# Performance work log

Measured on AMD Instinct MI355X. Metric: run time of the kernel, lower is better.

The kernel has to match this reference:

```python
import jax, jax.numpy as jnp
import numpy as np

B, S, H, L, V, T = 128, 512, 512, 2, 30, 64  # batch, enc len, hidden, layers, vocab, decode len


def _p(k, shape):
    return jax.random.normal(k, shape, jnp.float32) * 0.05


def setup_inputs() -> dict:
    key = jax.random.key(0)
    ks = jax.random.split(key, 24)
    inp = {"x": jax.random.normal(ks[0], (B, S, 2), jnp.float32)}
    inp["emb"] = _p(ks[1], (V, H))
    # encoder GRU (input dim 2 for layer 0, H for layer 1); PyTorch gate order r,z,n
    inp["enc_Wih0"] = _p(ks[2], (3 * H, 2));  inp["enc_Whh0"] = _p(ks[3], (3 * H, H))
    inp["enc_bih0"] = _p(ks[4], (3 * H,));    inp["enc_bhh0"] = _p(ks[5], (3 * H,))
    inp["enc_Wih1"] = _p(ks[6], (3 * H, H));  inp["enc_Whh1"] = _p(ks[7], (3 * H, H))
    inp["enc_bih1"] = _p(ks[8], (3 * H,));    inp["enc_bhh1"] = _p(ks[9], (3 * H,))
    # decoder GRU (input dim H)
    inp["dec_Wih0"] = _p(ks[10], (3 * H, H)); inp["dec_Whh0"] = _p(ks[11], (3 * H, H))
    inp["dec_bih0"] = _p(ks[12], (3 * H,));   inp["dec_bhh0"] = _p(ks[13], (3 * H,))
    inp["dec_Wih1"] = _p(ks[14], (3 * H, H)); inp["dec_Whh1"] = _p(ks[15], (3 * H, H))
    inp["dec_bih1"] = _p(ks[16], (3 * H,));   inp["dec_bhh1"] = _p(ks[17], (3 * H,))
    inp["fc_W"] = _p(ks[18], (V, 2 * H));     inp["fc_b"] = _p(ks[19], (V,))
    return inp


def gru_cell(xt, h, Wih, Whh, bih, bhh):
    gi = xt @ Wih.T + bih
    gh = h @ Whh.T + bhh
    i_r, i_z, i_n = jnp.split(gi, 3, axis=-1)
    h_r, h_z, h_n = jnp.split(gh, 3, axis=-1)
    r = jax.nn.sigmoid(i_r + h_r)
    z = jax.nn.sigmoid(i_z + h_z)
    n = jnp.tanh(i_n + r * h_n)
    return (1.0 - z) * n + z * h


def _forward(x, emb,
             enc_Wih0, enc_Whh0, enc_bih0, enc_bhh0,
             enc_Wih1, enc_Whh1, enc_bih1, enc_bhh1,
             dec_Wih0, dec_Whh0, dec_bih0, dec_bhh0,
             dec_Wih1, dec_Whh1, dec_bih1, dec_bhh1,
             fc_W, fc_b):
    b = x.shape[0]
    h0 = jnp.zeros((b, H), x.dtype)

    # ---- encoder: 2-layer GRU scanned over time ----
    def enc_step(hs, xt):
        a = gru_cell(xt, hs[0], enc_Wih0, enc_Whh0, enc_bih0, enc_bhh0)
        c = gru_cell(a, hs[1], enc_Wih1, enc_Whh1, enc_bih1, enc_bhh1)
        return (a, c), c

    (e0, e1), out_enc_t = jax.lax.scan(enc_step, (h0, h0), x.transpose(1, 0, 2))
    out_enc = out_enc_t.transpose(1, 0, 2)  # [B, S, H]

    def dec_step(carry, _):
        (d0, d1), tok = carry
        e = emb[tok]  # [B, H]
        n0 = gru_cell(e, d0, dec_Wih0, dec_Whh0, dec_bih0, dec_bhh0)
        n1 = gru_cell(n0, d1, dec_Wih1, dec_Whh1, dec_bih1, dec_bhh1)
        out_dec = n1  # [B, H]
        sim = jnp.einsum('bsh,bh->bs', out_enc, out_dec)  # [B, S]
        # faithful to nn.Softmax() implicit dim on 3-D [B,S,1] tensor -> dim=0 (batch)
        att_w = jax.nn.softmax(sim, axis=0)
        attention = jnp.einsum('bs,bsh->bh', att_w, out_enc)  # [B, H]
        logits = jnp.concatenate([out_dec, attention], axis=-1) @ fc_W.T + fc_b  # [B, V]
        tok_next = jnp.argmax(logits, axis=-1)
        return ((n0, n1), tok_next), logits

    tok0 = jnp.zeros((b,), jnp.int32)
    ((f0, f1), _), logits_t = jax.lax.scan(dec_step, ((e0, e1), tok0), None, length=T)
    vec_out = logits_t.transpose(1, 0, 2)  # [B, T, V]
    hidden = jnp.stack([f0, f1], axis=0)   # [n_layers, B, H]
    return vec_out, hidden


def reference(x, emb,
              enc_Wih0, enc_Whh0, enc_bih0, enc_bhh0,
              enc_Wih1, enc_Whh1, enc_bih1, enc_bhh1,
              dec_Wih0, dec_Whh0, dec_bih0, dec_bhh0,
              dec_Wih1, dec_Whh1, dec_bih1, dec_bhh1,
              fc_W, fc_b):
    return _forward(x, emb,
                    enc_Wih0, enc_Whh0, enc_bih0, enc_bhh0,
                    enc_Wih1, enc_Whh1, enc_bih1, enc_bhh1,
                    dec_Wih0, dec_Whh0, dec_bih0, dec_bhh0,
                    dec_Wih1, dec_Whh1, dec_bih1, dec_bhh1,
                    fc_W, fc_b)
```

## Files before the change

kernel.cpp:

```cpp
#include <hip/hip_runtime.h>
#include <math.h>

typedef short  s16x8 __attribute__((ext_vector_type(8)));
typedef float  f32x4 __attribute__((ext_vector_type(4)));
typedef unsigned short u16;
typedef unsigned long long u64;

#define MFMA16(a, b, c) __builtin_amdgcn_mfma_f32_16x16x32_bf16((a), (b), (c), 0, 0, 0)

#define BB 128
#define SS 512
#define HH 512
#define VV 30
#define TT 64

#define SC_SYS  __HIP_MEMORY_SCOPE_SYSTEM

__device__ __forceinline__ float b2f(u16 v) {
  union { unsigned int u; float f; } c; c.u = ((unsigned int)v) << 16; return c.f;
}
__device__ __forceinline__ u16 f2b(float f) {
  union { float f; unsigned int u; } c; c.f = f;
  unsigned int r = (c.u + 0x7FFFu + ((c.u >> 16) & 1u)) >> 16;
  return (u16)r;
}
__device__ __forceinline__ float sigm(float x) { return 1.f / (1.f + expf(-x)); }
__device__ __forceinline__ s16x8 ldf(const u16* p) { return *(const s16x8*)p; }

__device__ __forceinline__ u64  ld64c(const u64* p)      { return __hip_atomic_load(p, __ATOMIC_RELAXED, SC_SYS); }
__device__ __forceinline__ void st16c(u16* p, u16 v)     { __hip_atomic_store(p, v, __ATOMIC_RELAXED, SC_SYS); }
__device__ __forceinline__ void stf32c(float* p, float v){ __hip_atomic_store(p, v, __ATOMIC_RELAXED, SC_SYS); }
__device__ __forceinline__ float ldf32c(const float* p)  { return __hip_atomic_load(p, __ATOMIC_RELAXED, SC_SYS); }
__device__ __forceinline__ void sti32c(int* p, int v)    { __hip_atomic_store(p, v, __ATOMIC_RELAXED, SC_SYS); }
__device__ __forceinline__ int  ldi32c(const int* p)     { return __hip_atomic_load(p, __ATOMIC_RELAXED, SC_SYS); }

__device__ unsigned int g_cnt[8];
__device__ float g_smx[SS], g_ssum[SS];

#define C_L0 0
#define C_L1 1
#define C_G0 2
#define C_G1 3
#define C_SIM 4
#define C_SMX 5
#define C_ATT 6

__device__ __forceinline__ void waitp(int idx, int target) {
  if (target <= 0) return;
  unsigned long long t0 = __builtin_amdgcn_s_memrealtime();
  while ((int)__hip_atomic_load(&g_cnt[idx], __ATOMIC_RELAXED, SC_SYS) < target) {
    __builtin_amdgcn_s_sleep(1);
    if (__builtin_amdgcn_s_memrealtime() - t0 > (1ull << 21)) break;
  }
}
__device__ __forceinline__ void waitc2(int i1, int t1, int i2, int t2) {
  if (threadIdx.x == 0) { waitp(i1, t1); waitp(i2, t2); }
  __syncthreads();
}
__device__ __forceinline__ void waitc3(int i1, int t1, int i2, int t2, int i3, int t3) {
  if (threadIdx.x == 0) { waitp(i1, t1); waitp(i2, t2); waitp(i3, t3); }
  __syncthreads();
}
__device__ __forceinline__ void waitc4(int i1, int t1, int i2, int t2, int i3, int t3, int i4, int t4) {
  if (threadIdx.x == 0) { waitp(i1, t1); waitp(i2, t2); waitp(i3, t3); waitp(i4, t4); }
  __syncthreads();
}
__device__ __forceinline__ void arrive(int idx) {
  __syncthreads();
  if (threadIdx.x == 0) {
    asm volatile("s_waitcnt vmcnt(0) lgkmcnt(0)" ::: "memory");
    __hip_atomic_fetch_add(&g_cnt[idx], 1u, __ATOMIC_RELAXED, SC_SYS);
  }
}

__device__ __forceinline__ s16x8 ldl(const u16* SM, int row, int slot) {
  return *(const s16x8*)&SM[(row << 8) + ((slot ^ (row & 15)) << 3)];
}

__device__ __forceinline__ void stage64(u16* SMb, const u16* SRC, int mbase, int kc) {
  const int t = threadIdx.x;
  const u64* base = (const u64*)SRC;
  u64 v[16];
#pragma unroll
  for (int j = 0; j < 16; ++j) {
    const int g = kc * 8 + (j >> 1);
    const int half = j & 1;
    v[j] = ld64c(base + (size_t)(g * 128 + mbase + half * 32) * 8 + t);
  }
#pragma unroll
  for (int j = 0; j < 16; ++j) {
    const int gl = j >> 1, half = j & 1;
    const int row = half * 32 + (t >> 3);
    const int w = t & 7;
    const int s = ((w & 4) << 2) + 2 * gl + ((w >> 1) & 1);
    *(u64*)&SMb[(row << 8) + ((s ^ (row & 15)) << 3) + ((w & 1) << 2)] = v[j];
  }
}

__device__ __forceinline__ void stage128(u16* SM, const u16* SRC, int kc) {
  const int t = threadIdx.x;
  const u64* base = (const u64*)SRC;
  u64 v[32];
#pragma unroll
  for (int j = 0; j < 32; ++j) {
    const int g = kc * 8 + (j >> 2);
    const int q = j & 3;
    v[j] = ld64c(base + (size_t)(g * 128 + q * 32) * 8 + t);
  }
#pragma unroll
  for (int j = 0; j < 32; ++j) {
    const int gl = j >> 2, q = j & 3;
    const int row = q * 32 + (t >> 3);
    const int w = t & 7;
    const int s = ((w & 4) << 2) + 2 * gl + ((w >> 1) & 1);
    *(u64*)&SM[(row << 8) + ((s ^ (row & 15)) << 3) + ((w & 1) << 2)] = v[j];
  }
}


template <bool GATHER, bool COH_H>
__device__ __forceinline__ void gru_dual_staged(
    int bx, u16* SM,
    const u16* __restrict__ A1s, const int* __restrict__ gather,
    const u16* __restrict__ A2s,
    const u16* __restrict__ Wihs, const u16* __restrict__ Whhs,
    const float* __restrict__ bih, const float* __restrict__ bhh,
    float* __restrict__ hf, u16* __restrict__ hs_new,
    u16* __restrict__ oe, size_t oe_mstride)
{
  const int tid  = threadIdx.x;
  const int wave = tid >> 6, lane = tid & 63;
  const int lrow = lane & 15, lq = lane >> 4;
  const int gidx = bx >> 1;
  const int j0 = gidx * 16;
  const int mbase = (bx & 1) * 64;
  const int lr = wave * 16 + lrow;
  const int m0 = mbase + wave * 16;

  const u16* a1p = nullptr;
  if (GATHER)
    a1p = A1s + (size_t)ldi32c(&gather[m0 + lrow]) * 1024 + lq * 8;

  const u16* bp[6];
#pragma unroll
  for (int t = 0; t < 6; ++t) {
    int g = (t < 3) ? t : t - 3;
    const u16* W = (t < 3) ? Wihs : Whhs;
    bp[t] = W + (size_t)(g * HH + j0 + lrow) * 1024 + lq * 8;
  }

  f32x4 acc[6];
#pragma unroll
  for (int t = 0; t < 6; ++t) acc[t] = (f32x4){0.f, 0.f, 0.f, 0.f};

  for (int kc = 0; kc < 4; ++kc) {
    if (!GATHER) stage64(SM, A1s, mbase, kc);
    stage64(SM + 64 * 256, A2s, mbase, kc);
    __syncthreads();
#pragma unroll
    for (int ki = 0; ki < 4; ++ki) {
      const int sl = ki * 4 + lq;
      s16x8 a1h, a1l;
      if (GATHER) { a1h = ldf(a1p); a1l = ldf(a1p + 512); a1p += 32; }
      else        { a1h = ldl(SM, lr, sl); a1l = ldl(SM, lr, 16 + sl); }
      s16x8 a2h = ldl(SM, 64 + lr, sl), a2l = ldl(SM, 64 + lr, 16 + sl);
#pragma unroll
      for (int t = 0; t < 6; ++t) {
        s16x8 bh = ldf(bp[t]), bl = ldf(bp[t] + 512); bp[t] += 32;
        s16x8 ah = (t < 3) ? a1h : a2h;
        s16x8 al = (t < 3) ? a1l : a2l;
        acc[t] = MFMA16(ah, bh, acc[t]);
        acc[t] = MFMA16(ah, bl, acc[t]);
        acc[t] = MFMA16(al, bh, acc[t]);
      }
    }
    __syncthreads();
  }

  const int c = j0 + lrow;
  const float bir = bih[c], biz = bih[HH + c], bin = bih[2 * HH + c];
  const float bhr = bhh[c], bhz = bhh[HH + c], bhn = bhh[2 * HH + c];
#pragma unroll
  for (int r = 0; r < 4; ++r) {
    int m = mbase + wave * 16 + lq * 4 + r;
    float ir = acc[0][r] + bir, iz = acc[1][r] + biz, inn = acc[2][r] + bin;
    float hr = acc[3][r] + bhr, hz = acc[4][r] + bhz, hn = acc[5][r] + bhn;
    float rr = sigm(ir + hr);
    float zz = sigm(iz + hz);
    float nn = tanhf(inn + rr * hn);
    float hp = COH_H ? ldf32c(&hf[(size_t)m * HH + c]) : hf[(size_t)m * HH + c];
    float hv = (1.f - zz) * nn + zz * hp;
    if (COH_H) stf32c(&hf[(size_t)m * HH + c], hv);
    else       hf[(size_t)m * HH + c] = hv;
    u16 hi = f2b(hv);
    size_t cb = (size_t)(gidx * 128 + m) * 32 + lrow;
    st16c(&hs_new[cb], hi);
    st16c(&hs_new[cb + 16], f2b(hv - b2f(hi)));
    if (oe) oe[(size_t)m * oe_mstride + c] = hi;
  }
}

__device__ __forceinline__ void gru_l0_staged(
    int bx, int p, u16* SM,
    const float* __restrict__ x, const float* __restrict__ Wih0,
    const u16* __restrict__ Whh0s,
    const float* __restrict__ bih0, const float* __restrict__ bhh0,
    const u16* __restrict__ As,
    float* __restrict__ af, u16* __restrict__ as_new)
{
  const int tid  = threadIdx.x;
  const int wave = tid >> 6, lane = tid & 63;
  const int lrow = lane & 15, lq = lane >> 4;
  const int j0 = bx * 16;
  const int mw = wave * 32;
  const int r0 = mw + lrow, r1 = mw + 16 + lrow;

  const u16* bp[3];
#pragma unroll
  for (int t = 0; t < 3; ++t)
    bp[t] = Whh0s + (size_t)(t * HH + j0 + lrow) * 1024 + lq * 8;

  f32x4 acc[2][3];
#pragma unroll
  for (int i = 0; i < 2; ++i)
#pragma unroll
    for (int t = 0; t < 3; ++t) acc[i][t] = (f32x4){0.f, 0.f, 0.f, 0.f};

  for (int kc = 0; kc < 4; ++kc) {
    stage128(SM, As, kc);
    __syncthreads();
#pragma unroll
    for (int ki = 0; ki < 4; ++ki) {
      const int sl = ki * 4 + lq;
      s16x8 a0h = ldl(SM, r0, sl), a0l = ldl(SM, r0, 16 + sl);
      s16x8 a1h = ldl(SM, r1, sl), a1l = ldl(SM, r1, 16 + sl);
#pragma unroll
      for (int t = 0; t < 3; ++t) {
        s16x8 bh = ldf(bp[t]), bl = ldf(bp[t] + 512); bp[t] += 32;
        acc[0][t] = MFMA16(a0h, bh, acc[0][t]);
        acc[0][t] = MFMA16(a0h, bl, acc[0][t]);
        acc[0][t] = MFMA16(a0l, bh, acc[0][t]);
        acc[1][t] = MFMA16(a1h, bh, acc[1][t]);
        acc[1][t] = MFMA16(a1h, bl, acc[1][t]);
        acc[1][t] = MFMA16(a1l, bh, acc[1][t]);
      }
    }
    __syncthreads();
  }

  const int c = j0 + lrow;
  const float bir = bih0[c], biz = bih0[HH + c], bin = bih0[2 * HH + c];
  const float bhr = bhh0[c], bhz = bhh0[HH + c], bhn = bhh0[2 * HH + c];
  const float wr0 = Wih0[(size_t)c * 2],            wr1 = Wih0[(size_t)c * 2 + 1];
  const float wz0 = Wih0[(size_t)(HH + c) * 2],     wz1 = Wih0[(size_t)(HH + c) * 2 + 1];
  const float wn0 = Wih0[(size_t)(2 * HH + c) * 2], wn1 = Wih0[(size_t)(2 * HH + c) * 2 + 1];
#pragma unroll
  for (int tm = 0; tm < 2; ++tm) {
#pragma unroll
    for (int r = 0; r < 4; ++r) {
      int m = mw + tm * 16 + lq * 4 + r;
      float x0 = x[((size_t)m * SS + p) * 2];
      float x1 = x[((size_t)m * SS + p) * 2 + 1];
      float ir  = bir + x0 * wr0 + x1 * wr1;
      float iz  = biz + x0 * wz0 + x1 * wz1;
      float inn = bin + x0 * wn0 + x1 * wn1;
      float hr = acc[tm][0][r] + bhr, hz = acc[tm][1][r] + bhz, hn = acc[tm][2][r] + bhn;
      float rr = sigm(ir + hr);
      float zz = sigm(iz + hz);
      float nn = tanhf(inn + rr * hn);
      float hp = af[(size_t)m * HH + c];
      float hv = (1.f - zz) * nn + zz * hp;
      af[(size_t)m * HH + c] = hv;
      u16 hi = f2b(hv);
      size_t cb = (size_t)(bx * 128 + m) * 32 + lrow;
      st16c(&as_new[cb], hi);
      st16c(&as_new[cb + 16], f2b(hv - b2f(hi)));
    }
  }
}

__device__ __forceinline__ void sim_block(
    int bx, const float* __restrict__ n1f, const u16* __restrict__ oe,
    float* __restrict__ simt)
{
  const int b = bx >> 1, sc = bx & 1;
  const int wave = threadIdx.x >> 6, lane = threadIdx.x & 63;
  float xr[8];
  const u64* xp = (const u64*)(n1f + (size_t)b * HH + lane * 8);
#pragma unroll
  for (int j = 0; j < 4; ++j) {
    union { u64 q; float f[2]; } u; u.q = ld64c(xp + j);
    xr[2 * j] = u.f[0]; xr[2 * j + 1] = u.f[1];
  }
  int s0 = sc * 256 + wave * 64;
  for (int i = 0; i < 64; ++i) {
    int s = s0 + i;
    s16x8 ov = *(const s16x8*)(oe + ((size_t)b * SS + s) * HH + lane * 8);
    float acc = 0.f;
#pragma unroll
    for (int j = 0; j < 8; ++j) acc += xr[j] * b2f((u16)ov[j]);
    for (int off = 32; off; off >>= 1) acc += __shfl_down(acc, off);
    if (lane == 0) stf32c(&simt[(size_t)s * BB + b], acc);
  }
}

__device__ __forceinline__ void smax_block(int bx, const float* __restrict__ simt)
{
  const int wave = threadIdx.x >> 6, lane = threadIdx.x & 63;
  const int s = bx * 4 + wave;
  union { u64 q; float f[2]; } u;
  u.q = ld64c((const u64*)&simt[(size_t)s * BB + lane * 2]);
  float mx = fmaxf(u.f[0], u.f[1]);
  for (int off = 32; off; off >>= 1) mx = fmaxf(mx, __shfl_xor(mx, off));
  float e = expf(u.f[0] - mx) + expf(u.f[1] - mx);
  for (int off = 32; off; off >>= 1) e += __shfl_xor(e, off);
  if (lane == 0) { stf32c(&g_smx[s], mx); stf32c(&g_ssum[s], e); }
}

__device__ __forceinline__ void attn_block(
    int b, int tstep, const float* __restrict__ simt, const float* __restrict__ n1f,
    const u16* __restrict__ oe, const float* __restrict__ fcW,
    const float* __restrict__ fcb, float* __restrict__ dout,
    int* __restrict__ tok)
{
  __shared__ float wsm[SS];
  __shared__ float xv[2 * HH];
  __shared__ float lg[32];
  const int t = threadIdx.x;

  for (int s = t; s < SS; s += 256) {
    float sv = ldf32c(&simt[(size_t)s * BB + b]);
    float mx = ldf32c(&g_smx[s]);
    float sm = ldf32c(&g_ssum[s]);
    wsm[s] = expf(sv - mx) / sm;
  }
  xv[t]       = ldf32c(&n1f[(size_t)b * HH + t]);
  xv[t + 256] = ldf32c(&n1f[(size_t)b * HH + t + 256]);
  __syncthreads();

  {
    float a0 = 0.f, a1 = 0.f;
    const u16* base = oe + (size_t)b * SS * HH;
    for (int s = 0; s < SS; ++s) {
      float w = wsm[s];
      a0 += w * b2f(base[(size_t)s * HH + t]);
      a1 += w * b2f(base[(size_t)s * HH + t + 256]);
    }
    xv[HH + t]       = a0;
    xv[HH + t + 256] = a1;
  }
  __syncthreads();

  int wave = t >> 6, lane = t & 63;
  for (int v = wave; v < VV; v += 4) {
    const float* wr = fcW + (size_t)v * (2 * HH);
    float acc = 0.f;
#pragma unroll
    for (int i = 0; i < 16; ++i) acc += xv[i * 64 + lane] * wr[i * 64 + lane];
    for (int off = 32; off; off >>= 1) acc += __shfl_down(acc, off);
    if (lane == 0) {
      float lv = acc + fcb[v];
      lg[v] = lv;
      dout[(size_t)b * (TT * VV) + (size_t)tstep * VV + v] = lv;
    }
  }
  __syncthreads();

  if (t == 0) {
    float best = lg[0]; int bi = 0;
    for (int v = 1; v < VV; ++v) if (lg[v] > best) { best = lg[v]; bi = v; }
    sti32c(&tok[b], bi);
  }
}

__global__ __launch_bounds__(256) void enc_persist(
    const float* __restrict__ x, const float* __restrict__ Wih0,
    const u16* __restrict__ Whh0s,
    const float* __restrict__ bih0, const float* __restrict__ bhh0,
    const u16* __restrict__ Wih1s, const u16* __restrict__ Whh1s,
    const float* __restrict__ bih1, const float* __restrict__ bhh1,
    u16* ABF0, u16* ABF1, float* af,
    u16* CBF0, u16* CBF1, float* cf,
    u16* out_enc)
{
  __shared__ u16 SM[32768];
  const int bx = blockIdx.x;
  const u16* pa = ABF0; u16* pa_n = ABF1;
  const u16* pc = CBF0; u16* pc_n = CBF1;
  for (int p = 0; p <= SS; ++p) {
    waitc2(C_L0, 32 * p, C_L1, 64 * (p - 1));
    if (bx < 32) {
      if (p < SS) {
        gru_l0_staged(bx, p, SM, x, Wih0, Whh0s, bih0, bhh0, pa, af, pa_n);
        arrive(C_L0);
      }
    } else {
      if (p > 0) {
        u16* oe = out_enc + (size_t)(p - 1) * HH;
        gru_dual_staged<false, false>(bx - 32, SM, pa, nullptr, pc,
                                      Wih1s, Whh1s, bih1, bhh1,
                                      cf, pc_n, oe, (size_t)SS * HH);
        arrive(C_L1);
      }
    }
    const u16* tp;
    tp = pa; pa = pa_n; pa_n = (u16*)tp;
    tp = pc; pc = pc_n; pc_n = (u16*)tp;
  }
}

__global__ __launch_bounds__(256) void dec_persist(
    const u16* __restrict__ EMBs, int* tok,
    const u16* __restrict__ WdIH0, const u16* __restrict__ WdHH0,
    const float* __restrict__ dbih0, const float* __restrict__ dbhh0,
    const u16* __restrict__ WdIH1, const u16* __restrict__ WdHH1,
    const float* __restrict__ dbih1, const float* __restrict__ dbhh1,
    float* af, float* cf,
    u16* D0A, u16* D0B, u16* D1A, u16* D1B,
    const u16* __restrict__ oe, float* simt,
    const float* __restrict__ fcW, const float* __restrict__ fcb,
    float* dout)
{
  __shared__ u16 SM[32768];
  const int bx = blockIdx.x;
  const u16* d0c = D0A; u16* d0n = D0B;
  const u16* d1c = D1A; u16* d1n = D1B;
  for (int t = 0; t < TT; ++t) {
    if (bx < 64) {
      waitc3(C_G0, 64 * t, C_ATT, 128 * t, C_G1, 64 * (t - 1));
      gru_dual_staged<true, false>(bx, SM, EMBs, tok, d0c,
                                   WdIH0, WdHH0, dbih0, dbhh0, af, d0n,
                                   nullptr, 0);
      arrive(C_G0);
    }
    { const u16* tp = d0c; d0c = d0n; d0n = (u16*)tp; }

    if (bx < 64) {
      waitc4(C_G0, 64 * (t + 1), C_G1, 64 * t, C_SIM, 256 * t, C_ATT, 128 * t);
      gru_dual_staged<false, true>(bx, SM, d0c, nullptr, d1c,
                                   WdIH1, WdHH1, dbih1, dbhh1, cf, d1n,
                                   nullptr, 0);
      arrive(C_G1);
    }
    { const u16* tp = d1c; d1c = d1n; d1n = (u16*)tp; }

    waitc3(C_G1, 64 * (t + 1), C_SMX, 128 * t, C_ATT, 128 * t);
    sim_block(bx, cf, oe, simt);
    arrive(C_SIM);

    if (bx < 128) {
      waitc2(C_SIM, 256 * (t + 1), C_ATT, 128 * t);
      smax_block(bx, simt);
      arrive(C_SMX);
    }

    if (bx < BB) {
      waitc4(C_SMX, 128 * (t + 1), C_SIM, 256 * (t + 1),
             C_G1, 64 * (t + 1), C_G0, 64 * (t + 1));
      attn_block(bx, t, simt, cf, oe, fcW, fcb, dout, tok);
      arrive(C_ATT);
    }
  }
}

__global__ __launch_bounds__(256) void splitall(
    const float* __restrict__ s0, u16* d0, const float* __restrict__ s1, u16* d1,
    const float* __restrict__ s2, u16* d2, const float* __restrict__ s3, u16* d3,
    const float* __restrict__ s4, u16* d4, const float* __restrict__ s5, u16* d5,
    const float* __restrict__ s6, u16* d6, const float* __restrict__ s7, u16* d7)
{
  const int WN = 3 * HH * HH;
  int i = blockIdx.x * 256 + threadIdx.x;
  const float* s; u16* d; int j;
  if      (i < 1 * WN) { s = s0; d = d0; j = i; }
  else if (i < 2 * WN) { s = s1; d = d1; j = i - 1 * WN; }
  else if (i < 3 * WN) { s = s2; d = d2; j = i - 2 * WN; }
  else if (i < 4 * WN) { s = s3; d = d3; j = i - 3 * WN; }
  else if (i < 5 * WN) { s = s4; d = d4; j = i - 4 * WN; }
  else if (i < 6 * WN) { s = s5; d = d5; j = i - 5 * WN; }
  else if (i < 7 * WN) { s = s6; d = d6; j = i - 6 * WN; }
  else { j = i - 7 * WN; if (j >= VV * HH) return; s = s7; d = d7; }
  int r = j >> 9, k = j & 511;
  float v = s[j];
  u16 hi = f2b(v);
  d[(size_t)r * 1024 + k]       = hi;
  d[(size_t)r * 1024 + 512 + k] = f2b(v - b2f(hi));
}

__global__ __launch_bounds__(256) void initk(
    float* af, float* cf, u16* b0, u16* b1, u16* b2, u16* b3, int* tok)
{
  int i = blockIdx.x * 256 + threadIdx.x;
  b0[i] = 0; b1[i] = 0; b2[i] = 0; b3[i] = 0;
  if (i < BB * HH) { af[i] = 0.f; cf[i] = 0.f; }
  if (i < BB) tok[i] = 0;
  if (i < 8) g_cnt[i] = 0;
}

__global__ __launch_bounds__(256) void finalize(
    const float* __restrict__ d0, const float* __restrict__ d1,
    float* __restrict__ oh)
{
  int i = blockIdx.x * 256 + threadIdx.x;
  oh[i]           = d0[i];
  oh[BB * HH + i] = d1[i];
}

extern "C" void kernel_launch(void* const* d_in, const int* in_sizes, int n_in,
                              void* d_out, int out_size, void* d_ws, size_t ws_size,
                              hipStream_t stream) {
  const float* x     = (const float*)d_in[0];
  const float* emb   = (const float*)d_in[1];
  const float* eWih0 = (const float*)d_in[2];
  const float* eWhh0 = (const float*)d_in[3];
  const float* ebih0 = (const float*)d_in[4];
  const float* ebhh0 = (const float*)d_in[5];
  const float* eWih1 = (const float*)d_in[6];
  const float* eWhh1 = (const float*)d_in[7];
  const float* ebih1 = (const float*)d_in[8];
  const float* ebhh1 = (const float*)d_in[9];
  const float* dWih0 = (const float*)d_in[10];
  const float* dWhh0 = (const float*)d_in[11];
  const float* dbih0 = (const float*)d_in[12];
  const float* dbhh0 = (const float*)d_in[13];
  const float* dWih1 = (const float*)d_in[14];
  const float* dWhh1 = (const float*)d_in[15];
  const float* dbih1 = (const float*)d_in[16];
  const float* dbhh1 = (const float*)d_in[17];
  const float* fcW   = (const float*)d_in[18];
  const float* fcb   = (const float*)d_in[19];
  float* dout = (float*)d_out;

  char* wsb = (char*)d_ws;
  float* af   = (float*)(wsb + 0);
  float* cf   = (float*)(wsb + 262144);
  u16* ABF0   = (u16*)(wsb + 524288);
  u16* ABF1   = (u16*)(wsb + 786432);
  u16* CBF0   = (u16*)(wsb + 1048576);
  u16* CBF1   = (u16*)(wsb + 1310720);
  int* tok    = (int*)(wsb + 1572864);
  float* simt = (float*)(wsb + 1573376);
  u16* WeHH0  = (u16*)(wsb + 1835520);
  u16* WeIH1  = (u16*)(wsb + 4981248);
  u16* WeHH1  = (u16*)(wsb + 8126976);
  u16* WdIH0  = (u16*)(wsb + 11272704);
  u16* WdHH0  = (u16*)(wsb + 14418432);
  u16* WdIH1  = (u16*)(wsb + 17564160);
  u16* WdHH1  = (u16*)(wsb + 20709888);
  u16* EMBs   = (u16*)(wsb + 23855616);
  u16* oe     = (u16*)(wsb + 23917056);

  initk<<<512, 256, 0, stream>>>(af, cf, ABF0, ABF1, CBF0, CBF1, tok);

  splitall<<<21564, 256, 0, stream>>>(eWhh0, WeHH0, eWih1, WeIH1, eWhh1, WeHH1,
                                      dWih0, WdIH0, dWhh0, WdHH0, dWih1, WdIH1,
                                      dWhh1, WdHH1, emb, EMBs);

  enc_persist<<<96, 256, 0, stream>>>(x, eWih0, WeHH0, ebih0, ebhh0,
                                      WeIH1, WeHH1, ebih1, ebhh1,
                                      ABF0, ABF1, af, CBF0, CBF1, cf, oe);

  dec_persist<<<256, 256, 0, stream>>>(EMBs, tok, WdIH0, WdHH0, dbih0, dbhh0,
                                       WdIH1, WdHH1, dbih1, dbhh1,
                                       af, cf, ABF0, ABF1, CBF1, CBF0,
                                       oe, simt, fcW, fcb, dout);

  finalize<<<256, 256, 0, stream>>>(af, cf, dout + (size_t)BB * TT * VV);
}
```

Baseline: 25.75 ms.

## Double-buffer staged activations, coalesce hidden-state stores, widen layer-0 encoder tiles

```diff
diff --git a/kernel.cpp b/kernel.cpp
--- a/kernel.cpp
+++ b/kernel.cpp
@@ -28,11 +28,12 @@
 __device__ __forceinline__ s16x8 ldf(const u16* p) { return *(const s16x8*)p; }
 
 __device__ __forceinline__ u64  ld64c(const u64* p)      { return __hip_atomic_load(p, __ATOMIC_RELAXED, SC_SYS); }
-__device__ __forceinline__ void st16c(u16* p, u16 v)     { __hip_atomic_store(p, v, __ATOMIC_RELAXED, SC_SYS); }
+__device__ __forceinline__ void st64c(u64* p, u64 v)     { __hip_atomic_store(p, v, __ATOMIC_RELAXED, SC_SYS); }
 __device__ __forceinline__ void stf32c(float* p, float v){ __hip_atomic_store(p, v, __ATOMIC_RELAXED, SC_SYS); }
 __device__ __forceinline__ float ldf32c(const float* p)  { return __hip_atomic_load(p, __ATOMIC_RELAXED, SC_SYS); }
 __device__ __forceinline__ void sti32c(int* p, int v)    { __hip_atomic_store(p, v, __ATOMIC_RELAXED, SC_SYS); }
 __device__ __forceinline__ int  ldi32c(const int* p)     { return __hip_atomic_load(p, __ATOMIC_RELAXED, SC_SYS); }
+__device__ __forceinline__ void stf32(float* p, float v) { *p = v; }
 
 __device__ unsigned int g_cnt[8];
 __device__ float g_smx[SS], g_ssum[SS];
@@ -73,47 +74,44 @@
   }
 }
 
-__device__ __forceinline__ s16x8 ldl(const u16* SM, int row, int slot) {
-  return *(const s16x8*)&SM[(row << 8) + ((slot ^ (row & 15)) << 3)];
-}
-
-__device__ __forceinline__ void stage64(u16* SMb, const u16* SRC, int mbase, int kc) {
+__device__ __forceinline__ s16x8 ldl(const u16* buf, int row, int slot) {
+  return *(const s16x8*)&buf[(row << 8) + ((slot ^ (row & 15)) << 3)];
+}
+
+__device__ __forceinline__ void ldchunk64(u64* v, const u16* SRC, int mbase, int kc) {
   const int t = threadIdx.x;
   const u64* base = (const u64*)SRC;
-  u64 v[16];
+#pragma unroll
+  for (int j = 0; j < 16; ++j)
+    v[j] = ld64c(base + (size_t)((kc * 8 + (j >> 1)) * 128 + mbase + (j & 1) * 32) * 8 + t);
+}
+__device__ __forceinline__ void stchunk64(u16* buf, int rowoff, const u64* v) {
+  const int t = threadIdx.x;
 #pragma unroll
   for (int j = 0; j < 16; ++j) {
-    const int g = kc * 8 + (j >> 1);
-    const int half = j & 1;
-    v[j] = ld64c(base + (size_t)(g * 128 + mbase + half * 32) * 8 + t);
-  }
-#pragma unroll
-  for (int j = 0; j < 16; ++j) {
-    const int gl = j >> 1, half = j & 1;
-    const int row = half * 32 + (t >> 3);
+    const int gl = j >> 1;
+    const int row = rowoff + (j & 1) * 32 + (t >> 3);
     const int w = t & 7;
     const int s = ((w & 4) << 2) + 2 * gl + ((w >> 1) & 1);
-    *(u64*)&SMb[(row << 8) + ((s ^ (row & 15)) << 3) + ((w & 1) << 2)] = v[j];
-  }
-}
-
-__device__ __forceinline__ void stage128(u16* SM, const u16* SRC, int kc) {
+    *(u64*)&buf[(row << 8) + ((s ^ (row & 15)) << 3) + ((w & 1) << 2)] = v[j];
+  }
+}
+__device__ __forceinline__ void ldchunk128(u64* v, const u16* SRC, int kc) {
   const int t = threadIdx.x;
   const u64* base = (const u64*)SRC;
-  u64 v[32];
+#pragma unroll
+  for (int j = 0; j < 32; ++j)
+    v[j] = ld64c(base + (size_t)((kc * 8 + (j >> 2)) * 128 + (j & 3) * 32) * 8 + t);
+}
+__device__ __forceinline__ void stchunk128(u16* buf, const u64* v) {
+  const int t = threadIdx.x;
 #pragma unroll
   for (int j = 0; j < 32; ++j) {
-    const int g = kc * 8 + (j >> 2);
-    const int q = j & 3;
-    v[j] = ld64c(base + (size_t)(g * 128 + q * 32) * 8 + t);
-  }
-#pragma unroll
-  for (int j = 0; j < 32; ++j) {
-    const int gl = j >> 2, q = j & 3;
-    const int row = q * 32 + (t >> 3);
+    const int gl = j >> 2;
+    const int row = (j & 3) * 32 + (t >> 3);
     const int w = t & 7;
     const int s = ((w & 4) << 2) + 2 * gl + ((w >> 1) & 1);
-    *(u64*)&SM[(row << 8) + ((s ^ (row & 15)) << 3) + ((w & 1) << 2)] = v[j];
+    *(u64*)&buf[(row << 8) + ((s ^ (row & 15)) << 3) + ((w & 1) << 2)] = v[j];
   }
 }
 
@@ -153,17 +151,26 @@
 #pragma unroll
   for (int t = 0; t < 6; ++t) acc[t] = (f32x4){0.f, 0.f, 0.f, 0.f};
 
+  u64 v1[16], v2[16];
+  if (!GATHER) ldchunk64(v1, A1s, mbase, 0);
+  ldchunk64(v2, A2s, mbase, 0);
+  if (!GATHER) stchunk64(SM, 0, v1);
+  stchunk64(SM, 64, v2);
+  __syncthreads();
+
   for (int kc = 0; kc < 4; ++kc) {
-    if (!GATHER) stage64(SM, A1s, mbase, kc);
-    stage64(SM + 64 * 256, A2s, mbase, kc);
-    __syncthreads();
+    u16* buf = SM + ((kc & 1) << 15);
+    if (kc < 3) {
+      if (!GATHER) ldchunk64(v1, A1s, mbase, kc + 1);
+      ldchunk64(v2, A2s, mbase, kc + 1);
+    }
 #pragma unroll
     for (int ki = 0; ki < 4; ++ki) {
       const int sl = ki * 4 + lq;
       s16x8 a1h, a1l;
       if (GATHER) { a1h = ldf(a1p); a1l = ldf(a1p + 512); a1p += 32; }
-      else        { a1h = ldl(SM, lr, sl); a1l = ldl(SM, lr, 16 + sl); }
-      s16x8 a2h = ldl(SM, 64 + lr, sl), a2l = ldl(SM, 64 + lr, 16 + sl);
+      else        { a1h = ldl(buf, lr, sl); a1l = ldl(buf, lr, 16 + sl); }
+      s16x8 a2h = ldl(buf, 64 + lr, sl), a2l = ldl(buf, 64 + lr, 16 + sl);
 #pragma unroll
       for (int t = 0; t < 6; ++t) {
         s16x8 bh = ldf(bp[t]), bl = ldf(bp[t] + 512); bp[t] += 32;
@@ -174,7 +181,13 @@
         acc[t] = MFMA16(al, bh, acc[t]);
       }
     }
-    __syncthreads();
+    if (kc < 3) {
+      __syncthreads();
+      u16* nb = SM + (((kc + 1) & 1) << 15);
+      if (!GATHER) stchunk64(nb, 0, v1);
+      stchunk64(nb, 64, v2);
+      __syncthreads();
+    }
   }
 
   const int c = j0 + lrow;
@@ -191,12 +204,19 @@
     float hp = COH_H ? ldf32c(&hf[(size_t)m * HH + c]) : hf[(size_t)m * HH + c];
     float hv = (1.f - zz) * nn + zz * hp;
     if (COH_H) stf32c(&hf[(size_t)m * HH + c], hv);
-    else       hf[(size_t)m * HH + c] = hv;
+    else       stf32(&hf[(size_t)m * HH + c], hv);
     u16 hi = f2b(hv);
-    size_t cb = (size_t)(gidx * 128 + m) * 32 + lrow;
-    st16c(&hs_new[cb], hi);
-    st16c(&hs_new[cb + 16], f2b(hv - b2f(hi)));
+    int ml = m - mbase;
+    SM[ml * 32 + lrow]      = hi;
+    SM[ml * 32 + 16 + lrow] = f2b(hv - b2f(hi));
     if (oe) oe[(size_t)m * oe_mstride + c] = hi;
+  }
+  __syncthreads();
+  {
+    u64* dst = (u64*)hs_new + (size_t)(gidx * 128 + mbase) * 8;
+    const u64* src = (const u64*)SM;
+    st64c(dst + tid,       src[tid]);
+    st64c(dst + 256 + tid, src[256 + tid]);
   }
 }
 
@@ -211,49 +231,59 @@
   const int tid  = threadIdx.x;
   const int wave = tid >> 6, lane = tid & 63;
   const int lrow = lane & 15, lq = lane >> 4;
-  const int j0 = bx * 16;
+  const int j0 = bx * 32;
   const int mw = wave * 32;
   const int r0 = mw + lrow, r1 = mw + 16 + lrow;
 
-  const u16* bp[3];
-#pragma unroll
-  for (int t = 0; t < 3; ++t)
-    bp[t] = Whh0s + (size_t)(t * HH + j0 + lrow) * 1024 + lq * 8;
-
-  f32x4 acc[2][3];
+  const u16* bp[6];
+#pragma unroll
+  for (int u = 0; u < 6; ++u) {
+    int jg = u / 3, g = u % 3;
+    bp[u] = Whh0s + (size_t)(g * HH + j0 + jg * 16 + lrow) * 1024 + lq * 8;
+  }
+
+  f32x4 acc[2][2][3];
 #pragma unroll
   for (int i = 0; i < 2; ++i)
 #pragma unroll
-    for (int t = 0; t < 3; ++t) acc[i][t] = (f32x4){0.f, 0.f, 0.f, 0.f};
+    for (int jg = 0; jg < 2; ++jg)
+#pragma unroll
+      for (int g = 0; g < 3; ++g) acc[i][jg][g] = (f32x4){0.f, 0.f, 0.f, 0.f};
+
+  u64 v[32];
+  ldchunk128(v, As, 0);
+  stchunk128(SM, v);
+  __syncthreads();
 
   for (int kc = 0; kc < 4; ++kc) {
-    stage128(SM, As, kc);
-    __syncthreads();
+    u16* buf = SM + ((kc & 1) << 15);
+    if (kc < 3) ldchunk128(v, As, kc + 1);
 #pragma unroll
     for (int ki = 0; ki < 4; ++ki) {
       const int sl = ki * 4 + lq;
-      s16x8 a0h = ldl(SM, r0, sl), a0l = ldl(SM, r0, 16 + sl);
-      s16x8 a1h = ldl(SM, r1, sl), a1l = ldl(SM, r1, 16 + sl);
-#pragma unroll
-      for (int t = 0; t < 3; ++t) {
-        s16x8 bh = ldf(bp[t]), bl = ldf(bp[t] + 512); bp[t] += 32;
-        acc[0][t] = MFMA16(a0h, bh, acc[0][t]);
-        acc[0][t] = MFMA16(a0h, bl, acc[0][t]);
-        acc[0][t] = MFMA16(a0l, bh, acc[0][t]);
-        acc[1][t] = MFMA16(a1h, bh, acc[1][t]);
-        acc[1][t] = MFMA16(a1h, bl, acc[1][t]);
-        acc[1][t] = MFMA16(a1l, bh, acc[1][t]);
-      }
-    }
-    __syncthreads();
-  }
-
-  const int c = j0 + lrow;
-  const float bir = bih0[c], biz = bih0[HH + c], bin = bih0[2 * HH + c];
-  const float bhr = bhh0[c], bhz = bhh0[HH + c], bhn = bhh0[2 * HH + c];
-  const float wr0 = Wih0[(size_t)c * 2],            wr1 = Wih0[(size_t)c * 2 + 1];
-  const float wz0 = Wih0[(size_t)(HH + c) * 2],     wz1 = Wih0[(size_t)(HH + c) * 2 + 1];
-  const float wn0 = Wih0[(size_t)(2 * HH + c) * 2], wn1 = Wih0[(size_t)(2 * HH + c) * 2 + 1];
+      s16x8 a0h = ldl(buf, r0, sl), a0l = ldl(buf, r0, 16 + sl);
+      s16x8 a1h = ldl(buf, r1, sl), a1l = ldl(buf, r1, 16 + sl);
+#pragma unroll
+      for (int jg = 0; jg < 2; ++jg)
+#pragma unroll
+        for (int g = 0; g < 3; ++g) {
+          const u16* w = bp[jg * 3 + g];
+          s16x8 bh = ldf(w), bl = ldf(w + 512); bp[jg * 3 + g] = w + 32;
+          acc[0][jg][g] = MFMA16(a0h, bh, acc[0][jg][g]);
+          acc[0][jg][g] = MFMA16(a0h, bl, acc[0][jg][g]);
+          acc[0][jg][g] = MFMA16(a0l, bh, acc[0][jg][g]);
+          acc[1][jg][g] = MFMA16(a1h, bh, acc[1][jg][g]);
+          acc[1][jg][g] = MFMA16(a1h, bl, acc[1][jg][g]);
+          acc[1][jg][g] = MFMA16(a1l, bh, acc[1][jg][g]);
+        }
+    }
+    if (kc < 3) {
+      __syncthreads();
+      stchunk128(SM + (((kc + 1) & 1) << 15), v);
+      __syncthreads();
+    }
+  }
+
 #pragma unroll
   for (int tm = 0; tm < 2; ++tm) {
 #pragma unroll
@@ -261,20 +291,38 @@
       int m = mw + tm * 16 + lq * 4 + r;
       float x0 = x[((size_t)m * SS + p) * 2];
       float x1 = x[((size_t)m * SS + p) * 2 + 1];
-      float ir  = bir + x0 * wr0 + x1 * wr1;
-      float iz  = biz + x0 * wz0 + x1 * wz1;
-      float inn = bin + x0 * wn0 + x1 * wn1;
-      float hr = acc[tm][0][r] + bhr, hz = acc[tm][1][r] + bhz, hn = acc[tm][2][r] + bhn;
-      float rr = sigm(ir + hr);
-      float zz = sigm(iz + hz);
-      float nn = tanhf(inn + rr * hn);
-      float hp = af[(size_t)m * HH + c];
-      float hv = (1.f - zz) * nn + zz * hp;
-      af[(size_t)m * HH + c] = hv;
-      u16 hi = f2b(hv);
-      size_t cb = (size_t)(bx * 128 + m) * 32 + lrow;
-      st16c(&as_new[cb], hi);
-      st16c(&as_new[cb + 16], f2b(hv - b2f(hi)));
+#pragma unroll
+      for (int jg = 0; jg < 2; ++jg) {
+        const int c = j0 + jg * 16 + lrow;
+        const float bir = bih0[c], biz = bih0[HH + c], bin = bih0[2 * HH + c];
+        const float bhr = bhh0[c], bhz = bhh0[HH + c], bhn = bhh0[2 * HH + c];
+        float ir  = bir + x0 * Wih0[(size_t)c * 2]            + x1 * Wih0[(size_t)c * 2 + 1];
+        float iz  = biz + x0 * Wih0[(size_t)(HH + c) * 2]     + x1 * Wih0[(size_t)(HH + c) * 2 + 1];
+        float inn = bin + x0 * Wih0[(size_t)(2 * HH + c) * 2] + x1 * Wih0[(size_t)(2 * HH + c) * 2 + 1];
+        float hr = acc[tm][jg][0][r] + bhr;
+        float hz = acc[tm][jg][1][r] + bhz;
+        float hn = acc[tm][jg][2][r] + bhn;
+        float rr = sigm(ir + hr);
+        float zz = sigm(iz + hz);
+        float nn = tanhf(inn + rr * hn);
+        float hp = af[(size_t)m * HH + c];
+        float hv = (1.f - zz) * nn + zz * hp;
+        af[(size_t)m * HH + c] = hv;
+        u16 hi = f2b(hv);
+        SM[jg * 4096 + m * 32 + lrow]      = hi;
+        SM[jg * 4096 + m * 32 + 16 + lrow] = f2b(hv - b2f(hi));
+      }
+    }
+  }
+  __syncthreads();
+  {
+    const u64* src = (const u64*)SM;
+#pragma unroll
+    for (int jg = 0; jg < 2; ++jg) {
+      u64* dst = (u64*)as_new + (size_t)((2 * bx + jg) * 128) * 8;
+#pragma unroll
+      for (int k = 0; k < 4; ++k)
+        st64c(dst + k * 256 + tid, src[jg * 1024 + k * 256 + tid]);
     }
   }
 }
@@ -383,13 +431,13 @@
     u16* CBF0, u16* CBF1, float* cf,
     u16* out_enc)
 {
-  __shared__ u16 SM[32768];
+  __shared__ u16 SM[65536];
   const int bx = blockIdx.x;
   const u16* pa = ABF0; u16* pa_n = ABF1;
   const u16* pc = CBF0; u16* pc_n = CBF1;
   for (int p = 0; p <= SS; ++p) {
-    waitc2(C_L0, 32 * p, C_L1, 64 * (p - 1));
-    if (bx < 32) {
+    waitc2(C_L0, 16 * p, C_L1, 64 * (p - 1));
+    if (bx < 16) {
       if (p < SS) {
         gru_l0_staged(bx, p, SM, x, Wih0, Whh0s, bih0, bhh0, pa, af, pa_n);
         arrive(C_L0);
@@ -397,7 +445,7 @@
     } else {
       if (p > 0) {
         u16* oe = out_enc + (size_t)(p - 1) * HH;
-        gru_dual_staged<false, false>(bx - 32, SM, pa, nullptr, pc,
+        gru_dual_staged<false, false>(bx - 16, SM, pa, nullptr, pc,
                                       Wih1s, Whh1s, bih1, bhh1,
                                       cf, pc_n, oe, (size_t)SS * HH);
         arrive(C_L1);
@@ -421,7 +469,7 @@
     const float* __restrict__ fcW, const float* __restrict__ fcb,
     float* dout)
 {
-  __shared__ u16 SM[32768];
+  __shared__ u16 SM[65536];
   const int bx = blockIdx.x;
   const u16* d0c = D0A; u16* d0n = D0B;
   const u16* d1c = D1A; u16* d1n = D1B;
@@ -556,7 +604,7 @@
                                       dWih0, WdIH0, dWhh0, WdHH0, dWih1, WdIH1,
                                       dWhh1, WdHH1, emb, EMBs);
 
-  enc_persist<<<96, 256, 0, stream>>>(x, eWih0, WeHH0, ebih0, ebhh0,
+  enc_persist<<<80, 256, 0, stream>>>(x, eWih0, WeHH0, ebih0, ebhh0,
                                       WeIH1, WeHH1, ebih1, ebhh1,
                                       ABF0, ABF1, af, CBF0, CBF1, cf, oe);
 
```

Result: slower. 37.00 ms (+43.7%).
